# Performance work log

Hardware: AMD Instinct MI355X
Metric: run time of the kernel (lower is better)

Reference implementation:

```python
import jax, jax.numpy as jnp
import numpy as np

B, T, D, H, E = 32, 512, 768, 12, 6  # batch, seq(=input_size), n_embd, num_heads, per-head dim
DFF = 4 * D
EPS = 1e-5


def setup_inputs() -> dict:
    key = jax.random.key(0)
    ks = jax.random.split(key, 10)
    s = 0.02
    return {
        "x": jax.random.normal(ks[0], (B, T, D), jnp.float32),
        "Wq": jax.random.normal(ks[1], (H, D, E), jnp.float32) * s,
        "Wk": jax.random.normal(ks[2], (H, D, E), jnp.float32) * s,
        "Wv": jax.random.normal(ks[3], (H, D, E), jnp.float32) * s,
        "Wo": jax.random.normal(ks[4], (H * E, D), jnp.float32) * s,
        "bo": jnp.zeros((D,), jnp.float32),
        "W1": jax.random.normal(ks[5], (D, DFF), jnp.float32) * s,
        "b1": jnp.zeros((DFF,), jnp.float32),
        "W2": jax.random.normal(ks[6], (DFF, D), jnp.float32) * s,
        "b2": jnp.zeros((D,), jnp.float32),
        "g1": jnp.ones((D,), jnp.float32),
        "beta1": jnp.zeros((D,), jnp.float32),
        "g2": jnp.ones((D,), jnp.float32),
        "beta2": jnp.zeros((D,), jnp.float32),
    }


def _layernorm(x, g, b):
    m = jnp.mean(x, axis=-1, keepdims=True)
    v = jnp.var(x, axis=-1, keepdims=True)  # biased, matches torch LayerNorm
    return (x - m) * jax.lax.rsqrt(v + EPS) * g + b


def reference(x, Wq, Wk, Wv, Wo, bo, W1, b1, W2, b2, g1, beta1, g2, beta2):
    # --- pre-LN multi-head causal attention (dropout = identity, eval mode) ---
    xn = _layernorm(x, g1, beta1)
    q = jnp.einsum("btd,hde->bhte", xn, Wq)
    k = jnp.einsum("btd,hde->bhte", xn, Wk)
    v = jnp.einsum("btd,hde->bhte", xn, Wv)
    scores = jnp.einsum("bhte,bhse->bhts", q, k) * (E ** -0.5)
    causal = jnp.tril(jnp.ones((T, T), dtype=bool))
    scores = jnp.where(causal, scores, -jnp.inf)
    w = jax.nn.softmax(scores, axis=-1)
    o = jnp.einsum("bhts,bhse->bhte", w, v)
    o = o.transpose(0, 2, 1, 3).reshape(B, T, H * E)  # concat heads -> [B,T,72]
    x = x + o @ Wo + bo
    # --- pre-LN feed-forward ---
    y = _layernorm(x, g2, beta2)
    ff = jax.nn.relu(y @ W1 + b1) @ W2 + b2
    return x + ff
```

## Files before the change

kernel.cpp:

```cpp
#include <hip/hip_runtime.h>
#include <hip/hip_bf16.h>

#define BT 16384
#define DIM 768
#define NH 12
#define DFF 3072

typedef __attribute__((ext_vector_type(8))) short short8;
typedef __attribute__((ext_vector_type(4))) float floatx4;
typedef __attribute__((ext_vector_type(4))) unsigned short ushort4b;

using bf16 = __hip_bfloat16;

static __device__ __forceinline__ float b2f(bf16 v) { return __bfloat162float(v); }
static __device__ __forceinline__ bf16 f2b(float v) { return __float2bfloat16(v); }

static __device__ __forceinline__ void gload_lds16(const void* g, void* l) {
    __builtin_amdgcn_global_load_lds(
        (const __attribute__((address_space(1))) unsigned int*)g,
        (__attribute__((address_space(3))) unsigned int*)l, 16, 0, 0);
}

__global__ __launch_bounds__(256) void pack_small_kernel(
    const float* __restrict__ Wq, const float* __restrict__ Wk, const float* __restrict__ Wv,
    const float* __restrict__ Wo, bf16* __restrict__ wqkv, bf16* __restrict__ wo_t)
{
    int i = blockIdx.x * 256 + threadIdx.x;
    const int S0 = 256 * 768, S1 = 768 * 96;
    if (i < S0) {
        int c = i / 768, dd = i % 768;
        float v = 0.f;
        if (c < 216) {
            int sel = c / 72, cc = c % 72, h = cc / 6, e = cc % 6;
            const float* W = (sel == 0) ? Wq : (sel == 1) ? Wk : Wv;
            v = W[((size_t)h * 768 + dd) * 6 + e];
        }
        wqkv[i] = f2b(v);
    } else if ((i -= S0) < S1) {
        int n = i / 96, r = i % 96;
        wo_t[i] = f2b(r < 72 ? Wo[r * 768 + n] : 0.f);
    }
}

__global__ __launch_bounds__(256) void transpose_kernel(
    const float* __restrict__ in, bf16* __restrict__ out, int R, int C)
{
    __shared__ float t[32][33];
    int c0 = blockIdx.x * 32, r0 = blockIdx.y * 32;
    int cx = threadIdx.x & 31, ry = threadIdx.x >> 5;
#pragma unroll
    for (int j = 0; j < 4; j++)
        t[ry + j * 8][cx] = in[(size_t)(r0 + ry + j * 8) * C + c0 + cx];
    __syncthreads();
    int rx = cx, cy = ry;
#pragma unroll
    for (int j = 0; j < 4; j++)
        out[(size_t)(c0 + cy + j * 8) * R + r0 + rx] = f2b(t[rx][cy + j * 8]);
}

__global__ __launch_bounds__(192) void ln_kernel(
    const float* __restrict__ x, const float* __restrict__ g, const float* __restrict__ be,
    bf16* __restrict__ out)
{
    int row = blockIdx.x;
    int tid = threadIdx.x;
    const float4* xr = (const float4*)(x + (size_t)row * DIM);
    float4 v = xr[tid];
    float s = v.x + v.y + v.z + v.w;
    float s2 = v.x * v.x + v.y * v.y + v.z * v.z + v.w * v.w;
#pragma unroll
    for (int off = 32; off; off >>= 1) {
        s += __shfl_down(s, off);
        s2 += __shfl_down(s2, off);
    }
    __shared__ float red[6];
    int wv = tid >> 6, ln = tid & 63;
    if (ln == 0) { red[wv] = s; red[3 + wv] = s2; }
    __syncthreads();
    float ts = red[0] + red[1] + red[2];
    float ts2 = red[3] + red[4] + red[5];
    float mean = ts * (1.f / 768.f);
    float var = ts2 * (1.f / 768.f) - mean * mean;
    float rstd = rsqrtf(var + 1e-5f);
    int c = tid * 4;
    float o0 = (v.x - mean) * rstd * g[c + 0] + be[c + 0];
    float o1 = (v.y - mean) * rstd * g[c + 1] + be[c + 1];
    float o2 = (v.z - mean) * rstd * g[c + 2] + be[c + 2];
    float o3 = (v.w - mean) * rstd * g[c + 3] + be[c + 3];
    bf16 h0 = f2b(o0), h1 = f2b(o1), h2 = f2b(o2), h3 = f2b(o3);
    ushort4b pk;
    pk[0] = *(unsigned short*)&h0; pk[1] = *(unsigned short*)&h1;
    pk[2] = *(unsigned short*)&h2; pk[3] = *(unsigned short*)&h3;
    *(ushort4b*)(out + (size_t)row * DIM + c) = pk;
}

template <int NSLAB, bool RELU, bool BIAS, bool RES, bool BF16OUT>
__global__ __launch_bounds__(256) void gemm_kernel(
    const bf16* __restrict__ A, const bf16* __restrict__ Bt,
    const float* __restrict__ bias, const float* __restrict__ res,
    void* __restrict__ Cv, int M, int N, int K)
{
    constexpr int SMEM_BYTES = BF16OUT ? (128 * 136 * 2) : (NSLAB * 2 * 128 * 32 * 2);
    __shared__ __align__(16) char smem[SMEM_BYTES];
    bf16* lA = (bf16*)smem;
    bf16* lB = lA + NSLAB * 128 * 32;

    const int tid = threadIdx.x;
    const int bm = blockIdx.x * 128;
    const int bn = blockIdx.y * 128;
    const int wave = tid >> 6, lane = tid & 63;
    const int wm = (wave >> 1) * 64, wn = (wave & 1) * 64;
    const int quad = lane >> 4, l16 = lane & 15;
    const int lrow = lane >> 2;
    const int lkc = (lane & 3) * 8;

    floatx4 acc[4][4] = {};

    for (int k0 = 0; k0 < K; k0 += NSLAB * 32) {
#pragma unroll
        for (int s = 0; s < NSLAB; s++) {
#pragma unroll
            for (int it = 0; it < 2; it++) {
                int r = wave * 32 + it * 16;
                gload_lds16(A + (size_t)(bm + r + lrow) * K + k0 + s * 32 + lkc,
                            lA + s * 4096 + r * 32);
                gload_lds16(Bt + (size_t)(bn + r + lrow) * K + k0 + s * 32 + lkc,
                            lB + s * 4096 + r * 32);
            }
        }
        __syncthreads();
#pragma unroll
        for (int s = 0; s < NSLAB; s++) {
            short8 af[4], bfr[4];
#pragma unroll
            for (int mt = 0; mt < 4; mt++)
                af[mt] = *(const short8*)(lA + s * 4096 + (wm + mt * 16 + l16) * 32 + quad * 8);
#pragma unroll
            for (int nt = 0; nt < 4; nt++)
                bfr[nt] = *(const short8*)(lB + s * 4096 + (wn + nt * 16 + l16) * 32 + quad * 8);
#pragma unroll
            for (int mt = 0; mt < 4; mt++)
#pragma unroll
                for (int nt = 0; nt < 4; nt++)
                    acc[mt][nt] = __builtin_amdgcn_mfma_f32_16x16x32_bf16(af[mt], bfr[nt], acc[mt][nt], 0, 0, 0);
        }
        __syncthreads();
    }

    if constexpr (BF16OUT) {
        bf16* ltile = (bf16*)smem;
#pragma unroll
        for (int mt = 0; mt < 4; mt++) {
#pragma unroll
            for (int nt = 0; nt < 4; nt++) {
                int tc = wn + nt * 16 + l16;
#pragma unroll
                for (int r = 0; r < 4; r++) {
                    int tr = wm + mt * 16 + quad * 4 + r;
                    float v0 = acc[mt][nt][r];
                    if constexpr (BIAS) v0 += bias[bn + tc];
                    if constexpr (RELU) v0 = fmaxf(v0, 0.f);
                    ltile[tr * 136 + tc] = f2b(v0);
                }
            }
        }
        __syncthreads();
        bf16* C = (bf16*)Cv;
        int rr0 = tid >> 4, col8 = (tid & 15) * 8;
        int gc = bn + col8;
#pragma unroll
        for (int p = 0; p < 8; p++) {
            int rr = p * 16 + rr0;
            if (gc < N)
                *(short8*)(C + (size_t)(bm + rr) * N + gc) =
                    *(const short8*)(ltile + rr * 136 + col8);
        }
    } else {
        float* C = (float*)Cv;
#pragma unroll
        for (int mt = 0; mt < 4; mt++) {
#pragma unroll
            for (int nt = 0; nt < 4; nt++) {
                int gc = bn + wn + nt * 16 + l16;
                if (gc < N) {
#pragma unroll
                    for (int r = 0; r < 4; r++) {
                        int gr = bm + wm + mt * 16 + quad * 4 + r;
                        float v0 = acc[mt][nt][r];
                        if constexpr (BIAS) v0 += bias[gc];
                        if constexpr (RES) v0 += res[(size_t)gr * N + gc];
                        if constexpr (RELU) v0 = fmaxf(v0, 0.f);
                        C[(size_t)gr * N + gc] = v0;
                    }
                }
            }
        }
    }
}

__global__ __launch_bounds__(256) void attn_kernel(const bf16* __restrict__ qkv, bf16* __restrict__ o_pad)
{
    int blk = blockIdx.x;
    int half = blk & 1;
    int bh = blk >> 1;
    int b = bh / NH, h = bh % NH;
    int wave = threadIdx.x >> 6, lane = threadIdx.x & 63;
    const int jmap0[4] = {0, 2, 5, 7}, jmap1[4] = {1, 3, 4, 6};
    int j = half ? jmap1[wave] : jmap0[wave];
    int t = j * 64 + lane;
    int smax = half ? 448 : 512;

    __shared__ float ks[512 * 6];
    __shared__ float vs[512 * 6];
    const bf16* base = qkv + (size_t)b * 512 * 216;
    for (int i = threadIdx.x; i < smax * 6; i += 256) {
        int s = i / 6, e = i % 6;
        ks[i] = b2f(base[s * 216 + 72 + h * 6 + e]);
        vs[i] = b2f(base[s * 216 + 144 + h * 6 + e]);
    }
    __syncthreads();

    float q0 = b2f(base[t * 216 + h * 6 + 0]);
    float q1 = b2f(base[t * 216 + h * 6 + 1]);
    float q2 = b2f(base[t * 216 + h * 6 + 2]);
    float q3 = b2f(base[t * 216 + h * 6 + 3]);
    float q4 = b2f(base[t * 216 + h * 6 + 4]);
    float q5 = b2f(base[t * 216 + h * 6 + 5]);

    const float scale = 0.4082482904638630f;
    float m = -1e30f, l = 0.f;
    float o0 = 0, o1 = 0, o2 = 0, o3 = 0, o4 = 0, o5 = 0;
    for (int s = 0; s <= t; s++) {
        const float* kk = &ks[s * 6];
        float sc = (q0 * kk[0] + q1 * kk[1] + q2 * kk[2] + q3 * kk[3] + q4 * kk[4] + q5 * kk[5]) * scale;
        float nm = fmaxf(m, sc);
        float alpha = __expf(m - nm);
        float p = __expf(sc - nm);
        l = l * alpha + p;
        const float* vv = &vs[s * 6];
        o0 = o0 * alpha + p * vv[0];
        o1 = o1 * alpha + p * vv[1];
        o2 = o2 * alpha + p * vv[2];
        o3 = o3 * alpha + p * vv[3];
        o4 = o4 * alpha + p * vv[4];
        o5 = o5 * alpha + p * vv[5];
        m = nm;
    }
    float inv = 1.f / l;
    bf16* orow = o_pad + (size_t)(b * 512 + t) * 96 + h * 6;
    orow[0] = f2b(o0 * inv);
    orow[1] = f2b(o1 * inv);
    orow[2] = f2b(o2 * inv);
    orow[3] = f2b(o3 * inv);
    orow[4] = f2b(o4 * inv);
    orow[5] = f2b(o5 * inv);
}

extern "C" void kernel_launch(void* const* d_in, const int* in_sizes, int n_in,
                              void* d_out, int out_size, void* d_ws, size_t ws_size,
                              hipStream_t stream)
{
    const float* x   = (const float*)d_in[0];
    const float* Wq  = (const float*)d_in[1];
    const float* Wk  = (const float*)d_in[2];
    const float* Wv  = (const float*)d_in[3];
    const float* Wo  = (const float*)d_in[4];
    const float* bo  = (const float*)d_in[5];
    const float* W1  = (const float*)d_in[6];
    const float* b1  = (const float*)d_in[7];
    const float* W2  = (const float*)d_in[8];
    const float* b2  = (const float*)d_in[9];
    const float* g1  = (const float*)d_in[10];
    const float* be1 = (const float*)d_in[11];
    const float* g2  = (const float*)d_in[12];
    const float* be2 = (const float*)d_in[13];

    char* ws = (char*)d_ws;
    size_t off = 0;
    auto alloc = [&](size_t bytes) {
        void* p = ws + off;
        off = (off + bytes + 255) & ~(size_t)255;
        return p;
    };
    bf16*  xn    = (bf16*)alloc((size_t)BT * DIM * 2);
    bf16*  qkvb  = (bf16*)alloc((size_t)BT * 216 * 2);
    bf16*  o_pad = (bf16*)alloc((size_t)BT * 96 * 2);
    float* x1    = (float*)alloc((size_t)BT * DIM * 4);
    bf16*  ffb   = (bf16*)alloc((size_t)BT * DFF * 2);
    bf16*  wqkv  = (bf16*)alloc((size_t)256 * 768 * 2);
    bf16*  wo_t  = (bf16*)alloc((size_t)768 * 96 * 2);
    bf16*  w1t   = (bf16*)alloc((size_t)3072 * 768 * 2);
    bf16*  w2t   = (bf16*)alloc((size_t)768 * 3072 * 2);

    const int PACK_N = 256 * 768 + 768 * 96;
    pack_small_kernel<<<(PACK_N + 255) / 256, 256, 0, stream>>>(Wq, Wk, Wv, Wo, wqkv, wo_t);
    transpose_kernel<<<dim3(3072 / 32, 768 / 32), 256, 0, stream>>>(W1, w1t, 768, 3072);
    transpose_kernel<<<dim3(768 / 32, 3072 / 32), 256, 0, stream>>>(W2, w2t, 3072, 768);

    ln_kernel<<<BT, 192, 0, stream>>>(x, g1, be1, xn);
    gemm_kernel<2, false, false, false, true><<<dim3(128, 2), 256, 0, stream>>>(
        xn, wqkv, nullptr, nullptr, qkvb, BT, 216, 768);
    attn_kernel<<<32 * NH * 2, 256, 0, stream>>>(qkvb, o_pad);
    gemm_kernel<1, false, true, true, false><<<dim3(128, 6), 256, 0, stream>>>(
        o_pad, wo_t, bo, x, x1, BT, 768, 96);
    ln_kernel<<<BT, 192, 0, stream>>>(x1, g2, be2, xn);
    gemm_kernel<2, true, true, false, true><<<dim3(128, 24), 256, 0, stream>>>(
        xn, w1t, b1, nullptr, ffb, BT, 3072, 768);
    gemm_kernel<2, false, true, true, false><<<dim3(128, 6), 256, 0, stream>>>(
        ffb, w2t, b2, x1, (float*)d_out, BT, 768, 3072);
}
```

Baseline: 458.1 us.

## Add 256x128 tiled GEMM with staged coalesced epilogue for FFN layers

Adds a new GEMM kernel that gives each block a 256x128 output tile, so each wave computes a 64x128 sub-tile with 4x8 MFMA accumulators. Both FFN matmuls now use it. The larger tile raises arithmetic intensity per LDS load and cuts the number of blocks. Its epilogue stages each wave's results through LDS so global stores and residual loads are coalesced vector accesses. The older GEMM also takes N and K as template constants. The cost is heavier register pressure, which launch_bounds(256,2) caps, plus extra synchronisation in the epilogue.

```diff
diff --git a/kernel.cpp b/kernel.cpp
--- a/kernel.cpp
+++ b/kernel.cpp
@@ -94,13 +94,14 @@
     *(ushort4b*)(out + (size_t)row * DIM + c) = pk;
 }
 
-template <int NSLAB, bool RELU, bool BIAS, bool RES, bool BF16OUT>
+template <int N, int K, int NSLAB, bool RELU, bool BIAS, bool RES, bool BF16OUT>
 __global__ __launch_bounds__(256) void gemm_kernel(
     const bf16* __restrict__ A, const bf16* __restrict__ Bt,
     const float* __restrict__ bias, const float* __restrict__ res,
-    void* __restrict__ Cv, int M, int N, int K)
-{
-    constexpr int SMEM_BYTES = BF16OUT ? (128 * 136 * 2) : (NSLAB * 2 * 128 * 32 * 2);
+    void* __restrict__ Cv, int M)
+{
+    constexpr int STAGE = NSLAB * 2 * 128 * 32 * 2;
+    constexpr int SMEM_BYTES = BF16OUT ? (STAGE > 128 * 136 * 2 ? STAGE : 128 * 136 * 2) : STAGE;
     __shared__ __align__(16) char smem[SMEM_BYTES];
     bf16* lA = (bf16*)smem;
     bf16* lB = lA + NSLAB * 128 * 32;
@@ -195,6 +196,128 @@
                 }
             }
         }
+    }
+}
+
+template <int N, int K, bool RELU, bool BIAS, bool RES, bool BF16OUT>
+__global__ __launch_bounds__(256, 2) void gemm256_kernel(
+    const bf16* __restrict__ A, const bf16* __restrict__ Bt,
+    const float* __restrict__ bias, const float* __restrict__ res,
+    void* __restrict__ Cv, int M)
+{
+    __shared__ __align__(16) char smem[49152];
+    bf16* lA = (bf16*)smem;
+    bf16* lB = lA + 2 * 256 * 32;
+
+    const int tid = threadIdx.x;
+    const int bm = blockIdx.x * 256;
+    const int bn = blockIdx.y * 128;
+    const int wave = tid >> 6, lane = tid & 63;
+    const int quad = lane >> 4, l16 = lane & 15;
+    const int lrow = lane >> 2;
+    const int lkc = (lane & 3) * 8;
+
+    floatx4 acc[4][8] = {};
+
+    for (int k0 = 0; k0 < K; k0 += 64) {
+#pragma unroll
+        for (int s = 0; s < 2; s++) {
+#pragma unroll
+            for (int it = 0; it < 4; it++) {
+                int r = (wave * 4 + it) * 16;
+                gload_lds16(A + (size_t)(bm + r + lrow) * K + k0 + s * 32 + lkc,
+                            lA + s * 8192 + r * 32);
+            }
+#pragma unroll
+            for (int it = 0; it < 2; it++) {
+                int r = (wave * 2 + it) * 16;
+                gload_lds16(Bt + (size_t)(bn + r + lrow) * K + k0 + s * 32 + lkc,
+                            lB + s * 4096 + r * 32);
+            }
+        }
+        __syncthreads();
+#pragma unroll
+        for (int s = 0; s < 2; s++) {
+            short8 af[4], bfr[8];
+#pragma unroll
+            for (int mt = 0; mt < 4; mt++)
+                af[mt] = *(const short8*)(lA + s * 8192 + (wave * 64 + mt * 16 + l16) * 32 + quad * 8);
+#pragma unroll
+            for (int nt = 0; nt < 8; nt++)
+                bfr[nt] = *(const short8*)(lB + s * 4096 + (nt * 16 + l16) * 32 + quad * 8);
+#pragma unroll
+            for (int mt = 0; mt < 4; mt++)
+#pragma unroll
+                for (int nt = 0; nt < 8; nt++)
+                    acc[mt][nt] = __builtin_amdgcn_mfma_f32_16x16x32_bf16(af[mt], bfr[nt], acc[mt][nt], 0, 0, 0);
+        }
+        __syncthreads();
+    }
+
+    float bv[8];
+    if constexpr (BIAS) {
+#pragma unroll
+        for (int nt = 0; nt < 8; nt++) bv[nt] = bias[bn + nt * 16 + l16];
+    }
+#pragma unroll
+    for (int p = 0; p < 4; p++) {
+        if (wave == p) {
+            if constexpr (BF16OUT) {
+                bf16* tile = (bf16*)smem;
+#pragma unroll
+                for (int mt = 0; mt < 4; mt++)
+#pragma unroll
+                    for (int nt = 0; nt < 8; nt++)
+#pragma unroll
+                        for (int r = 0; r < 4; r++) {
+                            float v0 = acc[mt][nt][r];
+                            if constexpr (BIAS) v0 += bv[nt];
+                            if constexpr (RELU) v0 = fmaxf(v0, 0.f);
+                            tile[(mt * 16 + quad * 4 + r) * 136 + nt * 16 + l16] = f2b(v0);
+                        }
+            } else {
+                float* tile = (float*)smem;
+#pragma unroll
+                for (int mt = 0; mt < 4; mt++)
+#pragma unroll
+                    for (int nt = 0; nt < 8; nt++)
+#pragma unroll
+                        for (int r = 0; r < 4; r++) {
+                            float v0 = acc[mt][nt][r];
+                            if constexpr (BIAS) v0 += bv[nt];
+                            if constexpr (RELU) v0 = fmaxf(v0, 0.f);
+                            tile[(mt * 16 + quad * 4 + r) * 132 + nt * 16 + l16] = v0;
+                        }
+            }
+        }
+        __syncthreads();
+        if constexpr (BF16OUT) {
+            const bf16* tile = (const bf16*)smem;
+            bf16* C = (bf16*)Cv;
+            int col8 = (tid & 15) * 8, r0 = tid >> 4;
+#pragma unroll
+            for (int j = 0; j < 4; j++) {
+                int rr = j * 16 + r0;
+                *(short8*)(C + (size_t)(bm + p * 64 + rr) * N + bn + col8) =
+                    *(const short8*)(tile + rr * 136 + col8);
+            }
+        } else {
+            const float* tile = (const float*)smem;
+            float* C = (float*)Cv;
+            int col4 = (tid & 31) * 4, r0 = tid >> 5;
+#pragma unroll
+            for (int j = 0; j < 8; j++) {
+                int rr = j * 8 + r0;
+                float4 v = *(const float4*)(tile + rr * 132 + col4);
+                size_t gi = (size_t)(bm + p * 64 + rr) * N + bn + col4;
+                if constexpr (RES) {
+                    float4 rv = *(const float4*)(res + gi);
+                    v.x += rv.x; v.y += rv.y; v.z += rv.z; v.w += rv.w;
+                }
+                *(float4*)(C + gi) = v;
+            }
+        }
+        __syncthreads();
     }
 }
 
@@ -298,14 +421,14 @@
     transpose_kernel<<<dim3(768 / 32, 3072 / 32), 256, 0, stream>>>(W2, w2t, 3072, 768);
 
     ln_kernel<<<BT, 192, 0, stream>>>(x, g1, be1, xn);
-    gemm_kernel<2, false, false, false, true><<<dim3(128, 2), 256, 0, stream>>>(
-        xn, wqkv, nullptr, nullptr, qkvb, BT, 216, 768);
+    gemm_kernel<216, 768, 2, false, false, false, true><<<dim3(128, 2), 256, 0, stream>>>(
+        xn, wqkv, nullptr, nullptr, qkvb, BT);
     attn_kernel<<<32 * NH * 2, 256, 0, stream>>>(qkvb, o_pad);
-    gemm_kernel<1, false, true, true, false><<<dim3(128, 6), 256, 0, stream>>>(
-        o_pad, wo_t, bo, x, x1, BT, 768, 96);
+    gemm_kernel<768, 96, 1, false, true, true, false><<<dim3(128, 6), 256, 0, stream>>>(
+        o_pad, wo_t, bo, x, x1, BT);
     ln_kernel<<<BT, 192, 0, stream>>>(x1, g2, be2, xn);
-    gemm_kernel<2, true, true, false, true><<<dim3(128, 24), 256, 0, stream>>>(
-        xn, w1t, b1, nullptr, ffb, BT, 3072, 768);
-    gemm_kernel<2, false, true, true, false><<<dim3(128, 6), 256, 0, stream>>>(
-        ffb, w2t, b2, x1, (float*)d_out, BT, 768, 3072);
-}
+    gemm256_kernel<3072, 768, true, true, false, true><<<dim3(64, 24), 256, 0, stream>>>(
+        xn, w1t, b1, nullptr, ffb, BT);
+    gemm256_kernel<768, 3072, false, true, true, false><<<dim3(64, 6), 256, 0, stream>>>(
+        ffb, w2t, b2, x1, (float*)d_out, BT);
+}
```

After: 461.9 us. Within noise of the previous version (+0.8%).
